# Kernel tuning notes

Measured on AMD Instinct MI355X. Metric: run time of the kernel, lower is better.

The kernel has to match this reference:

```python
import jax, jax.numpy as jnp
import numpy as np

Nu, Nd = 40000, 20000          # users, drugs
FIN, HID, H = 128, 256, 4      # input feat, hidden_dim, heads
D = HID // H                   # per-head dim (64)
HAN_OUT, HD = 64, 16           # HANConv out_channels, per-head dim
E, ER = 80000, 80000           # edges per relation (main / refined graph)


def _seg_softmax(a, seg, num):
    # segment softmax over destination index, stable
    m = jax.ops.segment_max(a, seg, num_segments=num)
    ex = jnp.exp(a - m[seg])
    s = jax.ops.segment_sum(ex, seg, num_segments=num)
    return ex / (s[seg] + 1e-16)


def setup_inputs():
    key = jax.random.key(0)
    ks = iter(jax.random.split(key, 80))
    def nrm(shape, scale=0.05):
        return jax.random.normal(next(ks), shape, jnp.float32) * scale
    def edges(ns, nd, e):
        src = jax.random.randint(next(ks), (e,), 0, ns)
        dst = jax.random.randint(next(ks), (e,), 0, nd)
        return jnp.stack([src, dst]).astype(jnp.int32)
    return {
        'x_user': nrm((Nu, FIN), 1.0), 'x_drug': nrm((Nd, FIN), 1.0),
        'x_user_ref': nrm((Nu, FIN), 1.0),
        'ei_ud': edges(Nu, Nd, E), 'ei_du': edges(Nd, Nu, E), 'ei_uu': edges(Nu, Nu, E),
        'ei_r1': edges(Nu, Nu, ER), 'ei_r2': edges(Nu, Nu, ER),
        # HANConv params (refined graph, user-only)
        'W_han': nrm((FIN, HAN_OUT)), 'b_han': jnp.zeros((HAN_OUT,), jnp.float32),
        'a_src_r1': nrm((H, HD)), 'a_dst_r1': nrm((H, HD)),
        'a_src_r2': nrm((H, HD)), 'a_dst_r2': nrm((H, HD)),
        'Wk_sem': nrm((HAN_OUT, HAN_OUT)), 'bk_sem': jnp.zeros((HAN_OUT,), jnp.float32),
        'q_sem': nrm((HAN_OUT,)),
        # per-node-type input linears
        'W_in_user': nrm((FIN, HID)), 'b_in_user': jnp.zeros((HID,), jnp.float32),
        'W_in_drug': nrm((FIN, HID)), 'b_in_drug': jnp.zeros((HID,), jnp.float32),
        # HGTConv params
        'W_kqv_user': nrm((HID, 3 * HID)), 'b_kqv_user': jnp.zeros((3 * HID,), jnp.float32),
        'W_kqv_drug': nrm((HID, 3 * HID)), 'b_kqv_drug': jnp.zeros((3 * HID,), jnp.float32),
        'Wk_ud': nrm((H, D, D), 0.1), 'Wv_ud': nrm((H, D, D), 0.1), 'p_ud': jnp.ones((H,), jnp.float32),
        'Wk_du': nrm((H, D, D), 0.1), 'Wv_du': nrm((H, D, D), 0.1), 'p_du': jnp.ones((H,), jnp.float32),
        'Wk_uu': nrm((H, D, D), 0.1), 'Wv_uu': nrm((H, D, D), 0.1), 'p_uu': jnp.ones((H,), jnp.float32),
        'W_out_user': nrm((HID, HID)), 'b_out_user': jnp.zeros((HID,), jnp.float32),
        'W_out_drug': nrm((HID, HID)), 'b_out_drug': jnp.zeros((HID,), jnp.float32),
        'skip_user': jnp.array(1.0, jnp.float32), 'skip_drug': jnp.array(1.0, jnp.float32),
        # final fusion linear
        'W_fin': nrm((HID + HAN_OUT, HID)), 'b_fin': jnp.zeros((HID,), jnp.float32),
    }


def reference(x_user, x_drug, x_user_ref, ei_ud, ei_du, ei_uu, ei_r1, ei_r2,
              W_han, b_han, a_src_r1, a_dst_r1, a_src_r2, a_dst_r2,
              Wk_sem, bk_sem, q_sem,
              W_in_user, b_in_user, W_in_drug, b_in_drug,
              W_kqv_user, b_kqv_user, W_kqv_drug, b_kqv_drug,
              Wk_ud, Wv_ud, p_ud, Wk_du, Wv_du, p_du, Wk_uu, Wv_uu, p_uu,
              W_out_user, b_out_user, W_out_drug, b_out_drug,
              skip_user, skip_drug, W_fin, b_fin):
    # ---------- HANConv on refined graph (two user-user meta-paths) ----------
    h = (x_user_ref @ W_han + b_han).reshape(Nu, H, HD)
    outs = []
    for ei, a_s, a_d in ((ei_r1, a_src_r1, a_dst_r1), (ei_r2, a_src_r2, a_dst_r2)):
        s, d = ei[0], ei[1]
        al_s = (h * a_s).sum(-1)                      # [Nu,H]
        al_d = (h * a_d).sum(-1)
        al = jax.nn.leaky_relu(al_s[s] + al_d[d], 0.2)  # [ER,H]
        al = _seg_softmax(al, d, Nu)
        o = jax.ops.segment_sum(h[s] * al[:, :, None], d, num_segments=Nu)
        outs.append(jax.nn.relu(o.reshape(Nu, HAN_OUT)))
    outs = jnp.stack(outs)                            # [2,Nu,64]
    score = (q_sem * jnp.tanh(outs @ Wk_sem + bk_sem).mean(axis=1)).sum(-1)  # [2]
    sem = jax.nn.softmax(score, axis=0)
    x_ref_out = (sem[:, None, None] * outs).sum(0)    # [Nu,64]

    # ---------- per-node-type input projection + relu ----------
    xu = jax.nn.relu(x_user @ W_in_user + b_in_user)
    xd = jax.nn.relu(x_drug @ W_in_drug + b_in_drug)

    # ---------- HGTConv ----------
    kqv_u = xu @ W_kqv_user + b_kqv_user
    kqv_d = xd @ W_kqv_drug + b_kqv_drug
    ku, qu, vu = [t.reshape(-1, H, D) for t in jnp.split(kqv_u, 3, axis=1)]
    kd, qd, vd = [t.reshape(-1, H, D) for t in jnp.split(kqv_d, 3, axis=1)]
    q_all = jnp.concatenate([qu, qd], axis=0)         # dst offsets: user=0, drug=Nu
    src_feat = {'user': (ku, vu), 'drug': (kd, vd)}
    dst_off = {'user': 0, 'drug': Nu}
    edge_types = [('user', 'drug', ei_ud, Wk_ud, Wv_ud, p_ud),
                  ('drug', 'user', ei_du, Wk_du, Wv_du, p_du),
                  ('user', 'user', ei_uu, Wk_uu, Wv_uu, p_uu)]
    scale = 1.0 / np.sqrt(D).astype(np.float32)
    alphas, vals, dsts = [], [], []
    for st, dt, ei, Wk, Wv, p in edge_types:
        k_src, v_src = src_feat[st]
        kp = jnp.einsum('nhd,hde->nhe', k_src, Wk)    # relation-specific per-head transform
        vp = jnp.einsum('nhd,hde->nhe', v_src, Wv)
        s, d = ei[0], ei[1]
        gd = d + dst_off[dt]
        a = (q_all[gd] * kp[s]).sum(-1) * p[None, :] * scale  # [E,H]
        alphas.append(a); vals.append(vp[s]); dsts.append(gd)
    a = jnp.concatenate(alphas)
    v = jnp.concatenate(vals)
    gd = jnp.concatenate(dsts)
    a = _seg_softmax(a, gd, Nu + Nd)                  # softmax over all in-edges of each dst
    out = jax.ops.segment_sum(v * a[:, :, None], gd, num_segments=Nu + Nd)
    out = out.reshape(Nu + Nd, HID)
    ou, od = out[:Nu], out[Nu:]
    ou = jax.nn.gelu(ou, approximate=False) @ W_out_user + b_out_user
    od = jax.nn.gelu(od, approximate=False) @ W_out_drug + b_out_drug
    su = jax.nn.sigmoid(skip_user)
    sd = jax.nn.sigmoid(skip_drug)
    ou = su * ou + (1.0 - su) * xu
    od = sd * od + (1.0 - sd) * xd                    # drug branch (kept for fidelity)
    # ---------- fuse HGT user embedding with HAN refined embedding ----------
    x_emb = jnp.concatenate([ou, x_ref_out], axis=1) @ W_fin + b_fin
    return x_emb
```

## Files before the change

kernel.cpp:

```cpp
#include <hip/hip_runtime.h>
#include <hip/hip_bf16.h>

#define NU 40000
#define ND 20000
#define NUP 40192
#define NDP 20224
#define HIDC 256
#define NHEAD 4
#define NEDGE 80000
#define CHUNK 2048
#define NCH 20
#define AL4 (NU * 4)

typedef __attribute__((ext_vector_type(8))) short bf16x8;
typedef __attribute__((ext_vector_type(8))) unsigned short u16x8;
typedef __attribute__((ext_vector_type(4))) float f32x4;

static __device__ __forceinline__ float b2f(unsigned short u) {
  union { unsigned int u; float f; } x; x.u = (unsigned int)u << 16; return x.f;
}
static __device__ __forceinline__ unsigned short f2b(float f) {
  union { float f; unsigned int u; } x; x.f = f;
  unsigned int r = x.u + 0x7FFFu + ((x.u >> 16) & 1u);
  return (unsigned short)(r >> 16);
}

static __device__ __forceinline__ void gload_lds16(const void* g, void* l) {
  __builtin_amdgcn_global_load_lds((const __attribute__((address_space(1))) unsigned int*)g,
                                   (__attribute__((address_space(3))) unsigned int*)l, 16, 0, 0);
}

template<int ACT>
__global__ __launch_bounds__(512)
void gemm_bf16(const unsigned short* __restrict__ A,
               const unsigned short* __restrict__ Bt,
               const float* __restrict__ bias,
               float* __restrict__ Cf, int ldcf,
               unsigned short* __restrict__ Cb, int ldcb,
               int M, int N, int K, int Mblk,
               const float* __restrict__ skipp,
               const unsigned short* __restrict__ xprev,
               int halfRows,
               const unsigned short* __restrict__ Bt2,
               const float* __restrict__ bias2, int M2,
               const float* __restrict__ as1, const float* __restrict__ ad1,
               const float* __restrict__ as2, const float* __restrict__ ad2,
               float* __restrict__ alsd)
{
  __shared__ __attribute__((aligned(128))) unsigned char smem[49152];
  unsigned short* ldsA = (unsigned short*)smem;
  unsigned short* ldsB = ldsA + 16384;
  float* ldsE = (float*)smem;

  const int Nx = (N + 127) >> 7;
  const int S = Nx << 3;
  const int flat = blockIdx.x;
  const int jj = flat % S, kq = flat / S;
  const int bx = jj >> 3, by = (kq << 3) + (jj & 7);
  if (by >= Mblk) return;

  const int tid  = threadIdx.x;
  const int lane = tid & 63, wv = tid >> 6;
  const int row0 = by * 256, col0 = bx * 128;

  const unsigned short* Btu = Bt;
  const float* biasu = bias;
  int Mu = M;
  int cfoff = 0;
  if (row0 >= halfRows) { Btu = Bt2; biasu = bias2; Mu = M2; cfoff = 64; }

  const int rl = lane >> 3;
  const int sS = (lane & 7) ^ rl;

  const int lr = lane & 15, lk = lane >> 4;
  const int wr = wv >> 1, wc = wv & 1;
  const int swz = lr & 7;

  f32x4 acc[4][4] = {};

  for (int k0 = 0; k0 < K; k0 += 64) {
#pragma unroll
    for (int i = 0; i < 4; i++) {
      size_t ga = (size_t)(row0 + wv * 32 + i * 8 + rl) * K + k0 + sS * 8;
      gload_lds16(A + ga, ldsA + wv * 2048 + i * 512);
    }
#pragma unroll
    for (int i = 0; i < 2; i++) {
      size_t gb = (size_t)(col0 + wv * 16 + i * 8 + rl) * K + k0 + sS * 8;
      gload_lds16(Btu + gb, ldsB + wv * 1024 + i * 512);
    }
    __syncthreads();
#pragma unroll
    for (int half = 0; half < 2; half++) {
      const int k8 = half * 4 + lk;
      const int so = (k8 ^ swz) << 3;
      bf16x8 av[4], bv[4];
#pragma unroll
      for (int m = 0; m < 4; m++)
        av[m] = *(const bf16x8*)&ldsA[(wr * 64 + m * 16 + lr) * 64 + so];
#pragma unroll
      for (int n = 0; n < 4; n++)
        bv[n] = *(const bf16x8*)&ldsB[(wc * 64 + n * 16 + lr) * 64 + so];
#pragma unroll
      for (int m = 0; m < 4; m++)
#pragma unroll
        for (int n = 0; n < 4; n++)
          acc[m][n] = __builtin_amdgcn_mfma_f32_16x16x32_bf16(av[m], bv[n], acc[m][n], 0, 0, 0);
    }
    __syncthreads();
  }

  if (ACT == 2) {
    __shared__ float csum[64];
    if (tid < 64) csum[tid] = 0.f;
    __syncthreads();
#pragma unroll
    for (int n = 0; n < 4; n++) {
      int col = col0 + wc * 64 + n * 16 + lr;
      if (col < N) {
        float bi = biasu[col];
        float local = 0.f;
#pragma unroll
        for (int m = 0; m < 4; m++)
#pragma unroll
          for (int g = 0; g < 4; g++) {
            int row = row0 + wr * 64 + m * 16 + lk * 4 + g;
            if (row < Mu) local += tanhf(acc[m][n][g] + bi);
          }
        atomicAdd(&csum[col], local);
      }
    }
    __syncthreads();
    if (tid < 64) atomicAdd(&Cf[cfoff + tid], csum[tid]);
    return;
  }

  float su = 0.f;
  if (ACT == 3) su = 1.f / (1.f + expf(-skipp[0]));
  float bi[4];
#pragma unroll
  for (int n = 0; n < 4; n++) {
    int col = col0 + wc * 64 + n * 16 + lr;
    bi[n] = (col < N) ? biasu[col] : 0.f;
  }

#pragma unroll
  for (int ch = 0; ch < 4; ch++) {
    __syncthreads();
    if (wr == ch) {
#pragma unroll
      for (int m = 0; m < 4; m++)
#pragma unroll
        for (int n = 0; n < 4; n++) {
          int c = wc * 64 + n * 16 + lr;
          int wbase = c + 2 * (c >> 5);
#pragma unroll
          for (int g = 0; g < 4; g++) {
            int lrow = m * 16 + lk * 4 + g;
            ldsE[lrow * 134 + wbase] = acc[m][n][g] + bi[n];
          }
        }
    }
    __syncthreads();
#pragma unroll
    for (int i = 0; i < 2; i++) {
      int c = tid + i * 512;
      int lrow = c >> 4, cc = c & 15;
      int row = row0 + ch * 64 + lrow;
      int colb = cc * 8;
      int base = lrow * 134 + 8 * cc + 2 * (cc >> 2);
      float v[8];
#pragma unroll
      for (int q2 = 0; q2 < 4; q2++) {
        float2 tv = *(const float2*)&ldsE[base + 2 * q2];
        v[2 * q2] = tv.x; v[2 * q2 + 1] = tv.y;
      }
      if (ACT == 1) {
#pragma unroll
        for (int q = 0; q < 8; q++) v[q] = fmaxf(v[q], 0.f);
      }
      if (ACT == 3) {
        u16x8 xp = *(const u16x8*)(xprev + (size_t)row * 256 + col0 + colb);
#pragma unroll
        for (int q = 0; q < 8; q++) v[q] = su * v[q] + (1.f - su) * b2f(xp[q]);
      }
      if (ACT == 4) {
        if (colb < 64 && row < Mu) {
          int hh = colb >> 4;
          int o0 = colb & 15;
          float s1 = 0, d1 = 0, s2 = 0, d2 = 0;
#pragma unroll
          for (int q = 0; q < 8; q++) {
            float x = v[q];
            s1 += x * as1[hh * 16 + o0 + q];
            d1 += x * ad1[hh * 16 + o0 + q];
            s2 += x * as2[hh * 16 + o0 + q];
            d2 += x * ad2[hh * 16 + o0 + q];
          }
          s1 += __shfl_xor(s1, 1); d1 += __shfl_xor(d1, 1);
          s2 += __shfl_xor(s2, 1); d2 += __shfl_xor(d2, 1);
          if ((lane & 1) == 0) {
            size_t idx = (size_t)row * 4 + hh;
            alsd[idx]           = s1;
            alsd[AL4 + idx]     = d1;
            alsd[2 * AL4 + idx] = s2;
            alsd[3 * AL4 + idx] = d2;
          }
        }
      }
      if (Cb) {
        u16x8 o;
#pragma unroll
        for (int q = 0; q < 8; q++) o[q] = f2b(row < Mu ? v[q] : 0.f);
        *(u16x8*)(Cb + (size_t)row * ldcb + col0 + colb) = o;
      }
      if (Cf && row < Mu) {
        int col = col0 + colb;
        if (col < N)
          *(float4*)&Cf[(size_t)row * ldcf + col] = make_float4(v[0], v[1], v[2], v[3]);
        if (col + 4 < N)
          *(float4*)&Cf[(size_t)row * ldcf + col + 4] = make_float4(v[4], v[5], v[6], v[7]);
      }
    }
  }
}

__global__ __launch_bounds__(256)
void prep_all(const float* __restrict__ x_user, const float* __restrict__ x_drug,
              const float* __restrict__ x_user_ref,
              const float* __restrict__ W_in_user, const float* __restrict__ W_in_drug,
              const float* __restrict__ W_kqv_user, const float* __restrict__ W_kqv_drug,
              const float* __restrict__ W_out_user, const float* __restrict__ W_fin,
              const float* __restrict__ W_han, const float* __restrict__ Wk_sem,
              const float* __restrict__ Wk_uu, const float* __restrict__ Wv_uu,
              const float* __restrict__ Wk_du, const float* __restrict__ Wv_du,
              const float* __restrict__ b_kqv_user, const float* __restrict__ b_kqv_drug,
              unsigned short* __restrict__ xub, unsigned short* __restrict__ xdb,
              unsigned short* __restrict__ xrb,
              unsigned short* __restrict__ Btu_in, unsigned short* __restrict__ Btd_in,
              unsigned short* __restrict__ Btall_u, unsigned short* __restrict__ Btall_d,
              unsigned short* __restrict__ Bto, unsigned short* __restrict__ Btf,
              unsigned short* __restrict__ Bth, unsigned short* __restrict__ BtWk,
              float* __restrict__ ball_u, float* __restrict__ ball_d,
              int* __restrict__ cnt)
{
  __shared__ float sWh[4096];
  __shared__ float sWk[64][65];
  const int b = blockIdx.x;
  const int tid = threadIdx.x;

  if (b < 16) {
    int mat = b >> 2, hh = b & 3;
    const float* Wkqv; const float* Wh; unsigned short* Bt; int coloff;
    switch (mat) {
      case 0:  Wkqv = W_kqv_user; Wh = Wk_uu; Bt = Btall_u;          coloff = 0;   break;
      case 1:  Wkqv = W_kqv_user; Wh = Wv_uu; Bt = Btall_u + 131072; coloff = 512; break;
      case 2:  Wkqv = W_kqv_drug; Wh = Wk_du; Bt = Btall_d;          coloff = 0;   break;
      default: Wkqv = W_kqv_drug; Wh = Wv_du; Bt = Btall_d + 65536;  coloff = 512; break;
    }
    for (int i = tid; i < 4096; i += 256) sWh[i] = Wh[hh * 4096 + i];
    __syncthreads();
    for (int ct = 0; ct < 4; ct++) {
      for (int i = tid; i < 4096; i += 256) {
        int cl = i >> 6, d = i & 63;
        sWk[cl][d] = Wkqv[(size_t)(ct * 64 + cl) * 768 + coloff + hh * 64 + d];
      }
      __syncthreads();
      int cl = tid & 63, eg = tid >> 6;
      float acc[16] = {};
      for (int d = 0; d < 64; d++) {
        float w = sWk[cl][d];
#pragma unroll
        for (int e = 0; e < 16; e++) acc[e] += w * sWh[d * 64 + eg * 16 + e];
      }
#pragma unroll
      for (int e = 0; e < 16; e++)
        Bt[(size_t)(hh * 64 + eg * 16 + e) * 256 + ct * 64 + cl] = f2b(acc[e]);
      __syncthreads();
    }
    return;
  }
  if (b < 21) {
    int j = (b - 16) * 256 + tid;
    const float* bb; const float* Wh; float* outp; int coloff, e256;
    if (j < 256)       { outp = &ball_u[j];        bb = b_kqv_user; Wh = Wk_uu; coloff = 0;   e256 = j; }
    else if (j < 512)  { ball_u[j] = b_kqv_user[j]; return; }
    else if (j < 768)  { outp = &ball_u[j];        bb = b_kqv_user; Wh = Wv_uu; coloff = 512; e256 = j - 512; }
    else if (j < 1024) { outp = &ball_d[j - 768];  bb = b_kqv_drug; Wh = Wk_du; coloff = 0;   e256 = j - 768; }
    else               { outp = &ball_d[j - 768];  bb = b_kqv_drug; Wh = Wv_du; coloff = 512; e256 = j - 1024; }
    int hh = e256 >> 6, e = e256 & 63;
    float acc = 0.f;
    for (int d = 0; d < 64; d++)
      acc += bb[coloff + hh * 64 + d] * Wh[hh * 4096 + d * 64 + e];
    *outp = acc;
    return;
  }
  if (b < 139) {
    int u = (b - 21) * 256 + tid;
    int idx = u * 4;
    if (idx < 3 * NU) *(int4*)&cnt[idx] = make_int4(0, 0, 0, 0);
    return;
  }
  if (b < 1323) {
    size_t i = (size_t)(b - 139) * 256 + tid;
    const float* W; unsigned short* Bt; int ldw, coloff, K, N;
    if (i < 32768)       { W = W_in_user;  Bt = Btu_in;          ldw = 256; coloff = 0;   K = 128; N = 256; }
    else if (i < 65536)  { W = W_in_drug;  Bt = Btd_in;          ldw = 256; coloff = 0;   K = 128; N = 256; i -= 32768; }
    else if (i < 131072) { W = W_kqv_user; Bt = Btall_u + 65536; ldw = 768; coloff = 256; K = 256; N = 256; i -= 65536; }
    else if (i < 196608) { W = W_out_user; Bt = Bto;             ldw = 256; coloff = 0;   K = 256; N = 256; i -= 131072; }
    else if (i < 278528) { W = W_fin;      Bt = Btf;             ldw = 256; coloff = 0;   K = 320; N = 256; i -= 196608; }
    else if (i < 294912) { W = W_han;      Bt = Bth;             ldw = 64;  coloff = 0;   K = 128; N = 64;  i -= 278528; }
    else                 { W = Wk_sem;     Bt = BtWk;            ldw = 64;  coloff = 0;   K = 64;  N = 64;  i -= 294912; }
    int n = (int)(i / K), k = (int)(i - (size_t)n * K);
    Bt[i] = (n < N) ? f2b(W[(size_t)k * ldw + coloff + n]) : 0;
    return;
  }
  {
    int bc = b - 1323;
    const float* in; unsigned short* outp; int M; int bl;
    if (bc < 2512)      { in = x_user;     outp = xub; M = NU; bl = bc; }
    else if (bc < 3776) { in = x_drug;     outp = xdb; M = ND; bl = bc - 2512; }
    else                { in = x_user_ref; outp = xrb; M = NU; bl = bc - 3776; }
    size_t e0 = ((size_t)bl * 256 + tid) * 8;
    int r = (int)(e0 >> 7);
    u16x8 o;
    if (r < M) {
      float4 a = *(const float4*)(in + e0);
      float4 bb = *(const float4*)(in + e0 + 4);
      o[0] = f2b(a.x); o[1] = f2b(a.y); o[2] = f2b(a.z); o[3] = f2b(a.w);
      o[4] = f2b(bb.x); o[5] = f2b(bb.y); o[6] = f2b(bb.z); o[7] = f2b(bb.w);
    } else {
#pragma unroll
      for (int q = 0; q < 8; q++) o[q] = 0;
    }
    *(u16x8*)(outp + e0) = o;
  }
}

__global__ void hist_all(const int* __restrict__ ei_du, const int* __restrict__ ei_uu,
                         const int* __restrict__ ei_r1, const int* __restrict__ ei_r2,
                         int* __restrict__ cnt)
{
  int t = blockIdx.x * 256 + threadIdx.x;
  if (t >= NEDGE) return;
  const int* ei; int* c;
  switch (blockIdx.y) {
    case 0: ei = ei_du; c = cnt; break;
    case 1: ei = ei_uu; c = cnt; break;
    case 2: ei = ei_r1; c = cnt + NU; break;
    default: ei = ei_r2; c = cnt + 2 * NU; break;
  }
  atomicAdd(&c[ei[NEDGE + t]], 1);
}

__global__ __launch_bounds__(256)
void scan_partial(const int* __restrict__ cnt, int* __restrict__ csums)
{
  int b = blockIdx.x;
  int rel = b / NCH, ch = b - rel * NCH;
  const int* c = cnt + (size_t)rel * NU;
  int t = threadIdx.x;
  int i0 = ch * CHUNK + t * 8;
  int s = 0;
#pragma unroll
  for (int j = 0; j < 8; j++) { int i = i0 + j; if (i < NU) s += c[i]; }
  __shared__ int ps[256];
  ps[t] = s;
  __syncthreads();
  for (int d = 128; d > 0; d >>= 1) { if (t < d) ps[t] += ps[t + d]; __syncthreads(); }
  if (t == 0) csums[b] = ps[0];
}

__global__ void scan_mid(const int* __restrict__ csums, int* __restrict__ coffs,
                         int* __restrict__ rs, float* __restrict__ colpart2)
{
  int r = threadIdx.x;
  if (r < 128) colpart2[r] = 0.f;
  if (r >= 3) return;
  int run = 0;
  for (int ch = 0; ch < NCH; ch++) { coffs[r * NCH + ch] = run; run += csums[r * NCH + ch]; }
  rs[(size_t)r * NUP + NU] = run;
}

__global__ __launch_bounds__(256)
void scan_final(int* __restrict__ cnt, const int* __restrict__ coffs,
                int* __restrict__ rs)
{
  int b = blockIdx.x;
  int rel = b / NCH, ch = b - rel * NCH;
  int* c = cnt + (size_t)rel * NU;
  int* r = rs + (size_t)rel * NUP;
  int t = threadIdx.x;
  int i0 = ch * CHUNK + t * 8;
  int loc[8]; int s = 0;
#pragma unroll
  for (int j = 0; j < 8; j++) {
    int i = i0 + j;
    loc[j] = (i < NU) ? c[i] : 0;
    if (i < NU) c[i] = 0;
    s += loc[j];
  }
  __shared__ int ps[256];
  ps[t] = s;
  __syncthreads();
  for (int d = 1; d < 256; d <<= 1) {
    int o = (t >= d) ? ps[t - d] : 0;
    __syncthreads();
    ps[t] += o;
    __syncthreads();
  }
  int run = coffs[b] + ps[t] - s;
#pragma unroll
  for (int j = 0; j < 8; j++) { int i = i0 + j; if (i < NU) { r[i] = run; run += loc[j]; } }
}

__global__ void han_fill2(const int* __restrict__ ei1, const int* __restrict__ ei2,
                          const float* __restrict__ alsd,
                          const int* __restrict__ rs, int* __restrict__ cur,
                          int* __restrict__ esrc1, float* __restrict__ aev1,
                          int* __restrict__ esrc2, float* __restrict__ aev2)
{
  int t = blockIdx.x * 256 + threadIdx.x;
  if (t >= NEDGE * 4) return;
  int y = blockIdx.y;
  const int* ei = y ? ei2 : ei1;
  const float* als = alsd + (y ? 2 * AL4 : 0);
  const float* ald = alsd + (y ? 3 * AL4 : AL4);
  const int* rsp = rs + (size_t)(y ? 2 : 1) * NUP;
  int* curp = cur + (size_t)(y ? 2 : 1) * NU;
  int* esrc = y ? esrc2 : esrc1;
  float* aev = y ? aev2 : aev1;
  int e = t >> 2, hh = t & 3;
  int s = ei[e], d = ei[NEDGE + e];
  float al = als[s * 4 + hh] + ald[d * 4 + hh];
  al = (al >= 0.f) ? al : 0.2f * al;
  float ex = expf(al);
  int pos = 0;
  if (hh == 0) pos = rsp[d] + atomicAdd(&curp[d], 1);
  pos = __shfl(pos, (threadIdx.x & 63) & ~3, 64);
  aev[pos * 4 + hh] = ex;
  if (hh == 0) esrc[pos] = s;
}

__global__ __launch_bounds__(256)
void han_gather2(const int* __restrict__ rs,
                 const int* __restrict__ esrc1, const float* __restrict__ aev1,
                 const int* __restrict__ esrc2, const float* __restrict__ aev2,
                 const float* __restrict__ h,
                 unsigned short* __restrict__ obf1, unsigned short* __restrict__ obf2)
{
  int gid = blockIdx.x * 256 + threadIdx.x;
  int wid = gid >> 6, lane = gid & 63;
  if (wid >= NUP) return;
  int y = blockIdx.y;
  const int* rsp = rs + (size_t)(y ? 2 : 1) * NUP;
  const int* esrc = y ? esrc2 : esrc1;
  const float* aev = y ? aev2 : aev1;
  unsigned short* obf = y ? obf2 : obf1;
  int head = lane >> 4;
  int beg = 0, end = 0;
  if (wid < NU) { beg = rsp[wid]; end = rsp[wid + 1]; }
  float asum = 0.f;
  for (int i = beg; i < end; i++) asum += aev[i * 4 + head];
  float inv = 1.f / (asum + 1e-16f);
  float a = 0.f;
  for (int i = beg; i < end; i++)
    a += aev[i * 4 + head] * inv * h[(size_t)esrc[i] * 64 + lane];
  obf[(size_t)wid * 64 + lane] = f2b(fmaxf(a, 0.f));
}

__global__ void sem_final2(const float* __restrict__ colpart2,
                           const float* __restrict__ q_sem, float* __restrict__ semv)
{
  int t = threadIdx.x;
  int j = t & 63;
  __shared__ float sv[128];
  sv[t] = colpart2[t] * q_sem[j] * (1.0f / NU);
  __syncthreads();
  if (t == 0) {
    float s0 = 0, s1 = 0;
    for (int i = 0; i < 64; i++) { s0 += sv[i]; s1 += sv[64 + i]; }
    float m = fmaxf(s0, s1);
    float e0 = expf(s0 - m), e1 = expf(s1 - m);
    semv[0] = e0 / (e0 + e1); semv[1] = e1 / (e0 + e1);
  }
}

__global__ void hgt_fill2(const int* __restrict__ ei_du, const int* __restrict__ ei_uu,
                          const unsigned short* __restrict__ qb,
                          const unsigned short* __restrict__ kvdb,
                          const float* __restrict__ p_du, const float* __restrict__ p_uu,
                          const int* __restrict__ rs, int* __restrict__ cur,
                          int* __restrict__ esrc, float* __restrict__ aev)
{
  int t = blockIdx.x * 256 + threadIdx.x;
  if (t >= NEDGE * 4) return;
  int y = blockIdx.y;
  const int* ei = y ? ei_uu : ei_du;
  const unsigned short* kb = y ? qb : kvdb;
  const int ks = y ? 768 : 512;
  const int voff = y ? 512 : NUP * 768 + 256;
  const float* p = y ? p_uu : p_du;
  int e = t >> 2, hh = t & 3;
  int s = ei[e], d = ei[NEDGE + e];
  const uint4* qv = (const uint4*)(qb + (size_t)d * 768 + 256 + hh * 64);
  const uint4* kv = (const uint4*)(kb + (size_t)s * ks + hh * 64);
  float acc = 0.f;
#pragma unroll
  for (int i = 0; i < 8; i++) {
    uint4 a = qv[i], b = kv[i];
    unsigned int aw[4] = {a.x, a.y, a.z, a.w};
    unsigned int bw[4] = {b.x, b.y, b.z, b.w};
#pragma unroll
    for (int u = 0; u < 4; u++) {
      acc += b2f((unsigned short)(aw[u] & 0xffff)) * b2f((unsigned short)(bw[u] & 0xffff));
      acc += b2f((unsigned short)(aw[u] >> 16))    * b2f((unsigned short)(bw[u] >> 16));
    }
  }
  float ex = expf(acc * p[hh] * 0.125f);
  int pos = 0;
  if (hh == 0) pos = rs[d] + atomicAdd(&cur[d], 1);
  pos = __shfl(pos, (threadIdx.x & 63) & ~3, 64);
  aev[pos * 4 + hh] = ex;
  if (hh == 0) esrc[pos] = voff + s * ks;
}

__global__ __launch_bounds__(256)
void hgt_gather(const int* __restrict__ rs, const int* __restrict__ esrc,
                const float* __restrict__ aev, const unsigned short* __restrict__ vbase,
                unsigned short* __restrict__ houtb)
{
  int gid = blockIdx.x * 256 + threadIdx.x;
  int wid = gid >> 6, lane = gid & 63;
  if (wid >= NUP) return;
  int head = lane >> 4;
  int beg = 0, end = 0;
  if (wid < NU) { beg = rs[wid]; end = rs[wid + 1]; }
  float asum = 0.f;
  for (int i = beg; i < end; i++) asum += aev[i * 4 + head];
  float inv = 1.f / (asum + 1e-16f);
  float a0 = 0, a1 = 0, a2 = 0, a3 = 0;
  for (int i = beg; i < end; i++) {
    float w = aev[i * 4 + head] * inv;
    const ushort4 v = *(const ushort4*)(vbase + (size_t)esrc[i] + lane * 4);
    a0 += b2f(v.x) * w; a1 += b2f(v.y) * w; a2 += b2f(v.z) * w; a3 += b2f(v.w) * w;
  }
  ushort4 o;
  o.x = f2b(0.5f * a0 * (1.f + erff(a0 * 0.70710678118654752f)));
  o.y = f2b(0.5f * a1 * (1.f + erff(a1 * 0.70710678118654752f)));
  o.z = f2b(0.5f * a2 * (1.f + erff(a2 * 0.70710678118654752f)));
  o.w = f2b(0.5f * a3 * (1.f + erff(a3 * 0.70710678118654752f)));
  *(ushort4*)(houtb + (size_t)wid * 256 + lane * 4) = o;
}

__global__ void fill_ref_b(const unsigned short* __restrict__ obf1,
                           const unsigned short* __restrict__ obf2,
                           const float* __restrict__ semv, unsigned short* __restrict__ afinb)
{
  int t = blockIdx.x * 256 + threadIdx.x;
  if (t >= NUP * 64) return;
  int n = t >> 6, j = t & 63;
  float v = semv[0] * b2f(obf1[t]) + semv[1] * b2f(obf2[t]);
  afinb[(size_t)n * 320 + 256 + j] = f2b(v);
}

extern "C" void kernel_launch(void* const* d_in, const int* in_sizes, int n_in,
                              void* d_out, int out_size, void* d_ws, size_t ws_size,
                              hipStream_t stream)
{
  (void)in_sizes; (void)n_in; (void)out_size; (void)ws_size;
  const float* x_user     = (const float*)d_in[0];
  const float* x_drug     = (const float*)d_in[1];
  const float* x_user_ref = (const float*)d_in[2];
  const int*   ei_du      = (const int*)d_in[4];
  const int*   ei_uu      = (const int*)d_in[5];
  const int*   ei_r1      = (const int*)d_in[6];
  const int*   ei_r2      = (const int*)d_in[7];
  const float* W_han      = (const float*)d_in[8];
  const float* b_han      = (const float*)d_in[9];
  const float* a_src_r1   = (const float*)d_in[10];
  const float* a_dst_r1   = (const float*)d_in[11];
  const float* a_src_r2   = (const float*)d_in[12];
  const float* a_dst_r2   = (const float*)d_in[13];
  const float* Wk_sem     = (const float*)d_in[14];
  const float* bk_sem     = (const float*)d_in[15];
  const float* q_sem      = (const float*)d_in[16];
  const float* W_in_user  = (const float*)d_in[17];
  const float* b_in_user  = (const float*)d_in[18];
  const float* W_in_drug  = (const float*)d_in[19];
  const float* b_in_drug  = (const float*)d_in[20];
  const float* W_kqv_user = (const float*)d_in[21];
  const float* b_kqv_user = (const float*)d_in[22];
  const float* W_kqv_drug = (const float*)d_in[23];
  const float* b_kqv_drug = (const float*)d_in[24];
  const float* Wk_du      = (const float*)d_in[28];
  const float* Wv_du      = (const float*)d_in[29];
  const float* p_du       = (const float*)d_in[30];
  const float* Wk_uu      = (const float*)d_in[31];
  const float* Wv_uu      = (const float*)d_in[32];
  const float* p_uu       = (const float*)d_in[33];
  const float* W_out_user = (const float*)d_in[34];
  const float* b_out_user = (const float*)d_in[35];
  const float* skip_user  = (const float*)d_in[38];
  const float* W_fin      = (const float*)d_in[40];
  const float* b_fin      = (const float*)d_in[41];
  float* out = (float*)d_out;

  char* base = (char*)d_ws;
  size_t off = 0;
  auto alloc = [&](size_t bytes) { char* p = base + off; off += (bytes + 255) & ~(size_t)255; return p; };

  float* h       = (float*)alloc((size_t)NU * 64 * 4);
  float* alsd    = (float*)alloc((size_t)4 * AL4 * 4);
  float* colpart2= (float*)alloc(128 * 4);
  float* semv    = (float*)alloc(64);
  float* ball_u  = (float*)alloc(768 * 4);
  float* ball_d  = (float*)alloc(512 * 4);

  int* cnt   = (int*)alloc((size_t)3 * NU * 4);
  int* rs    = (int*)alloc((size_t)3 * NUP * 4);
  int* csums = (int*)alloc((size_t)3 * NCH * 4);
  int* coffs = (int*)alloc((size_t)3 * NCH * 4);
  int* esrcH = (int*)alloc((size_t)2 * NEDGE * 4);
  float* aevH= (float*)alloc((size_t)2 * NEDGE * 4 * 4);
  int* esrc1 = (int*)alloc((size_t)NEDGE * 4);
  float* aev1= (float*)alloc((size_t)NEDGE * 4 * 4);
  int* esrc2 = (int*)alloc((size_t)NEDGE * 4);
  float* aev2= (float*)alloc((size_t)NEDGE * 4 * 4);

  unsigned short* obf1 = (unsigned short*)alloc((size_t)NUP * 64 * 2);
  unsigned short* obf2 = (unsigned short*)alloc((size_t)NUP * 64 * 2);

  unsigned short* qukvb = (unsigned short*)alloc((size_t)NUP * 768 * 2);
  unsigned short* kvdb  = (unsigned short*)alloc((size_t)NDP * 512 * 2);

  unsigned short* xub2d = (unsigned short*)alloc((size_t)NUP * 256 * 2);
  unsigned short* xdb2d = (unsigned short*)alloc((size_t)NDP * 256 * 2);

  unsigned short* houtb = (unsigned short*)alloc((size_t)NUP * 256 * 2);
  unsigned short* xrb   = houtb;

  unsigned short* afinb = (unsigned short*)alloc((size_t)NUP * 320 * 2);
  unsigned short* xub   = afinb;
  unsigned short* xdb   = afinb + (size_t)NUP * 128;

  unsigned short* Btu_in  = (unsigned short*)alloc(256 * 128 * 2);
  unsigned short* Btd_in  = (unsigned short*)alloc(256 * 128 * 2);
  unsigned short* Btall_u = (unsigned short*)alloc(768 * 256 * 2);
  unsigned short* Btall_d = (unsigned short*)alloc(512 * 256 * 2);
  unsigned short* Bto     = (unsigned short*)alloc(256 * 256 * 2);
  unsigned short* Btf     = (unsigned short*)alloc(256 * 320 * 2);
  unsigned short* Bth     = (unsigned short*)alloc(128 * 128 * 2);
  unsigned short* BtWk    = (unsigned short*)alloc(128 * 64 * 2);

  dim3 blk(256), blk5(512);
  auto g1 = [](size_t n) { return dim3((unsigned)((n + 255) / 256)); };
  auto gg = [](int N, int Mblk) {
    int Nx = (N + 127) / 128;
    return dim3((unsigned)(((Mblk + 7) / 8) * 8 * Nx));
  };
  const int BIG = 1 << 30;
  const unsigned short* NB = nullptr;
  const float* NF = nullptr;

  const int prep_blocks = 16 + 5 + 118 + 1184 + 6288;
  prep_all<<<dim3(prep_blocks), blk, 0, stream>>>(
      x_user, x_drug, x_user_ref, W_in_user, W_in_drug, W_kqv_user, W_kqv_drug,
      W_out_user, W_fin, W_han, Wk_sem, Wk_uu, Wv_uu, Wk_du, Wv_du,
      b_kqv_user, b_kqv_drug,
      xub, xdb, xrb, Btu_in, Btd_in, Btall_u, Btall_d, Bto, Btf, Bth, BtWk,
      ball_u, ball_d, cnt);

  hist_all<<<dim3((NEDGE + 255) / 256, 4), blk, 0, stream>>>(ei_du, ei_uu, ei_r1, ei_r2, cnt);
  scan_partial<<<3 * NCH, blk, 0, stream>>>(cnt, csums);
  scan_mid<<<1, 128, 0, stream>>>(csums, coffs, rs, colpart2);
  scan_final<<<3 * NCH, blk, 0, stream>>>(cnt, coffs, rs);

  gemm_bf16<4><<<gg(64, 157), blk5, 0, stream>>>(
      xrb, Bth, b_han, h, 64, (unsigned short*)nullptr, 0, NU, 64, 128, 157,
      nullptr, nullptr, BIG, NB, NF, 0,
      a_src_r1, a_dst_r1, a_src_r2, a_dst_r2, alsd);

  han_fill2<<<dim3((NEDGE * 4 + 255) / 256, 2), blk, 0, stream>>>(
      ei_r1, ei_r2, alsd, rs, cnt, esrc1, aev1, esrc2, aev2);
  han_gather2<<<dim3((NUP * 64 + 255) / 256, 2), blk, 0, stream>>>(
      rs, esrc1, aev1, esrc2, aev2, h, obf1, obf2);

  gemm_bf16<2><<<gg(64, 314), blk5, 0, stream>>>(
      obf1, BtWk, bk_sem, colpart2, 0, (unsigned short*)nullptr, 0, NU, 64, 64, 314,
      nullptr, nullptr, NUP, BtWk, bk_sem, NUP + NU,
      NF, NF, NF, NF, nullptr);
  sem_final2<<<1, 128, 0, stream>>>(colpart2, q_sem, semv);

  gemm_bf16<1><<<gg(256, 236), blk5, 0, stream>>>(
      xub, Btu_in, b_in_user, (float*)nullptr, 0, xub2d, 256, NU, 256, 128, 236,
      nullptr, nullptr, NUP, Btd_in, b_in_drug, NUP + ND,
      NF, NF, NF, NF, nullptr);

  gemm_bf16<0><<<gg(768, 157), blk5, 0, stream>>>(
      xub2d, Btall_u, ball_u, (float*)nullptr, 0, qukvb, 768, NU, 768, 256, 157,
      nullptr, nullptr, BIG, NB, NF, 0, NF, NF, NF, NF, nullptr);
  gemm_bf16<0><<<gg(512, 79), blk5, 0, stream>>>(
      xdb2d, Btall_d, ball_d, (float*)nullptr, 0, kvdb, 512, ND, 512, 256, 79,
      nullptr, nullptr, BIG, NB, NF, 0, NF, NF, NF, NF, nullptr);

  hgt_fill2<<<dim3((NEDGE * 4 + 255) / 256, 2), blk, 0, stream>>>(
      ei_du, ei_uu, qukvb, kvdb, p_du, p_uu, rs, cnt, esrcH, aevH);
  hgt_gather<<<g1((size_t)NUP * 64), blk, 0, stream>>>(rs, esrcH, aevH, qukvb, houtb);

  gemm_bf16<3><<<gg(256, 157), blk5, 0, stream>>>(
      houtb, Bto, b_out_user, (float*)nullptr, 0, afinb, 320, NU, 256, 256, 157,
      skip_user, xub2d, BIG, NB, NF, 0, NF, NF, NF, NF, nullptr);
  fill_ref_b<<<g1((size_t)NUP * 64), blk, 0, stream>>>(obf1, obf2, semv, afinb);

  gemm_bf16<0><<<gg(256, 157), blk5, 0, stream>>>(
      afinb, Btf, b_fin, out, 256, (unsigned short*)nullptr, 0, NU, 256, 320, 157,
      nullptr, nullptr, BIG, NB, NF, 0, NF, NF, NF, NF, nullptr);
}
```

Measured before the change: 302.6 us.

## Merge user/drug KQV GEMMs and fuse HAN/HGT fill and gather kernels

The user and drug KQV projection GEMMs now run in one grouped launch: blocks beyond the first grid's count switch to the second problem's pointers and sizes. The HAN and HGT edge-fill kernels are merged into one 4-slice launch, and their gather kernels into one 3-slice launch. The semantic GEMM is moved after the gathers. This cuts the number of kernel launches and lets independent work share the GPU instead of running one small grid after another. In exchange the GEMM carries extra parameters and branches, and the merged kernels have divergent per-slice paths.

```diff
diff --git a/kernel.cpp b/kernel.cpp
--- a/kernel.cpp
+++ b/kernel.cpp
@@ -45,27 +45,45 @@
                const float* __restrict__ bias2, int M2,
                const float* __restrict__ as1, const float* __restrict__ ad1,
                const float* __restrict__ as2, const float* __restrict__ ad2,
-               float* __restrict__ alsd)
+               float* __restrict__ alsd,
+               int B1,
+               const unsigned short* __restrict__ A_r2,
+               const unsigned short* __restrict__ Bt_r2,
+               const float* __restrict__ bias_r2,
+               unsigned short* __restrict__ Cb_r2, int ldcb_r2,
+               int M_r2, int N_r2, int Mblk_r2)
 {
   __shared__ __attribute__((aligned(128))) unsigned char smem[49152];
   unsigned short* ldsA = (unsigned short*)smem;
   unsigned short* ldsB = ldsA + 16384;
   float* ldsE = (float*)smem;
 
-  const int Nx = (N + 127) >> 7;
+  int flat = blockIdx.x;
+  const unsigned short* Ap = A;
+  const unsigned short* Btp = Bt;
+  const float* biasp = bias;
+  float* Cfp = Cf;
+  unsigned short* Cbp = Cb;
+  int ldcbp = ldcb, Mp = M, Np = N, Mblkp = Mblk;
+  if (flat >= B1) {
+    flat -= B1;
+    Ap = A_r2; Btp = Bt_r2; biasp = bias_r2; Cbp = Cb_r2; ldcbp = ldcb_r2;
+    Mp = M_r2; Np = N_r2; Mblkp = Mblk_r2; Cfp = nullptr;
+  }
+
+  const int Nx = (Np + 127) >> 7;
   const int S = Nx << 3;
-  const int flat = blockIdx.x;
   const int jj = flat % S, kq = flat / S;
   const int bx = jj >> 3, by = (kq << 3) + (jj & 7);
-  if (by >= Mblk) return;
+  if (by >= Mblkp) return;
 
   const int tid  = threadIdx.x;
   const int lane = tid & 63, wv = tid >> 6;
   const int row0 = by * 256, col0 = bx * 128;
 
-  const unsigned short* Btu = Bt;
-  const float* biasu = bias;
-  int Mu = M;
+  const unsigned short* Btu = Btp;
+  const float* biasu = biasp;
+  int Mu = Mp;
   int cfoff = 0;
   if (row0 >= halfRows) { Btu = Bt2; biasu = bias2; Mu = M2; cfoff = 64; }
 
@@ -82,7 +100,7 @@
 #pragma unroll
     for (int i = 0; i < 4; i++) {
       size_t ga = (size_t)(row0 + wv * 32 + i * 8 + rl) * K + k0 + sS * 8;
-      gload_lds16(A + ga, ldsA + wv * 2048 + i * 512);
+      gload_lds16(Ap + ga, ldsA + wv * 2048 + i * 512);
     }
 #pragma unroll
     for (int i = 0; i < 2; i++) {
@@ -117,7 +135,7 @@
 #pragma unroll
     for (int n = 0; n < 4; n++) {
       int col = col0 + wc * 64 + n * 16 + lr;
-      if (col < N) {
+      if (col < Np) {
         float bi = biasu[col];
         float local = 0.f;
 #pragma unroll
@@ -131,7 +149,7 @@
       }
     }
     __syncthreads();
-    if (tid < 64) atomicAdd(&Cf[cfoff + tid], csum[tid]);
+    if (tid < 64) atomicAdd(&Cfp[cfoff + tid], csum[tid]);
     return;
   }
 
@@ -141,7 +159,7 @@
 #pragma unroll
   for (int n = 0; n < 4; n++) {
     int col = col0 + wc * 64 + n * 16 + lr;
-    bi[n] = (col < N) ? biasu[col] : 0.f;
+    bi[n] = (col < Np) ? biasu[col] : 0.f;
   }
 
 #pragma unroll
@@ -208,18 +226,18 @@
           }
         }
       }
-      if (Cb) {
+      if (Cbp) {
         u16x8 o;
 #pragma unroll
         for (int q = 0; q < 8; q++) o[q] = f2b(row < Mu ? v[q] : 0.f);
-        *(u16x8*)(Cb + (size_t)row * ldcb + col0 + colb) = o;
-      }
-      if (Cf && row < Mu) {
+        *(u16x8*)(Cbp + (size_t)row * ldcbp + col0 + colb) = o;
+      }
+      if (Cfp && row < Mu) {
         int col = col0 + colb;
-        if (col < N)
-          *(float4*)&Cf[(size_t)row * ldcf + col] = make_float4(v[0], v[1], v[2], v[3]);
-        if (col + 4 < N)
-          *(float4*)&Cf[(size_t)row * ldcf + col + 4] = make_float4(v[4], v[5], v[6], v[7]);
+        if (col < Np)
+          *(float4*)&Cfp[(size_t)row * ldcf + col] = make_float4(v[0], v[1], v[2], v[3]);
+        if (col + 4 < Np)
+          *(float4*)&Cfp[(size_t)row * ldcf + col + 4] = make_float4(v[4], v[5], v[6], v[7]);
       }
     }
   }
@@ -414,59 +432,117 @@
   for (int j = 0; j < 8; j++) { int i = i0 + j; if (i < NU) { r[i] = run; run += loc[j]; } }
 }
 
-__global__ void han_fill2(const int* __restrict__ ei1, const int* __restrict__ ei2,
-                          const float* __restrict__ alsd,
-                          const int* __restrict__ rs, int* __restrict__ cur,
-                          int* __restrict__ esrc1, float* __restrict__ aev1,
-                          int* __restrict__ esrc2, float* __restrict__ aev2)
+__global__ void fill_all(const int* __restrict__ ei_r1, const int* __restrict__ ei_r2,
+                         const int* __restrict__ ei_du, const int* __restrict__ ei_uu,
+                         const float* __restrict__ alsd,
+                         const unsigned short* __restrict__ qb,
+                         const unsigned short* __restrict__ kvdb,
+                         const float* __restrict__ p_du, const float* __restrict__ p_uu,
+                         const int* __restrict__ rs, int* __restrict__ cur,
+                         int* __restrict__ esrc1, float* __restrict__ aev1,
+                         int* __restrict__ esrc2, float* __restrict__ aev2,
+                         int* __restrict__ esrcH, float* __restrict__ aevH)
 {
   int t = blockIdx.x * 256 + threadIdx.x;
   if (t >= NEDGE * 4) return;
   int y = blockIdx.y;
-  const int* ei = y ? ei2 : ei1;
-  const float* als = alsd + (y ? 2 * AL4 : 0);
-  const float* ald = alsd + (y ? 3 * AL4 : AL4);
-  const int* rsp = rs + (size_t)(y ? 2 : 1) * NUP;
-  int* curp = cur + (size_t)(y ? 2 : 1) * NU;
-  int* esrc = y ? esrc2 : esrc1;
-  float* aev = y ? aev2 : aev1;
   int e = t >> 2, hh = t & 3;
-  int s = ei[e], d = ei[NEDGE + e];
-  float al = als[s * 4 + hh] + ald[d * 4 + hh];
-  al = (al >= 0.f) ? al : 0.2f * al;
-  float ex = expf(al);
-  int pos = 0;
-  if (hh == 0) pos = rsp[d] + atomicAdd(&curp[d], 1);
-  pos = __shfl(pos, (threadIdx.x & 63) & ~3, 64);
-  aev[pos * 4 + hh] = ex;
-  if (hh == 0) esrc[pos] = s;
+  if (y < 2) {
+    const int* ei = y ? ei_r2 : ei_r1;
+    const float* als = alsd + (y ? 2 * AL4 : 0);
+    const float* ald = alsd + (y ? 3 * AL4 : AL4);
+    const int* rsp = rs + (size_t)(y ? 2 : 1) * NUP;
+    int* curp = cur + (size_t)(y ? 2 : 1) * NU;
+    int* esrc = y ? esrc2 : esrc1;
+    float* aev = y ? aev2 : aev1;
+    int s = ei[e], d = ei[NEDGE + e];
+    float al = als[s * 4 + hh] + ald[d * 4 + hh];
+    al = (al >= 0.f) ? al : 0.2f * al;
+    float ex = expf(al);
+    int pos = 0;
+    if (hh == 0) pos = rsp[d] + atomicAdd(&curp[d], 1);
+    pos = __shfl(pos, (threadIdx.x & 63) & ~3, 64);
+    aev[pos * 4 + hh] = ex;
+    if (hh == 0) esrc[pos] = s;
+  } else {
+    int yy = y - 2;
+    const int* ei = yy ? ei_uu : ei_du;
+    const unsigned short* kb = yy ? qb : kvdb;
+    const int ks = yy ? 768 : 512;
+    const int voff = yy ? 512 : NUP * 768 + 256;
+    const float* p = yy ? p_uu : p_du;
+    int s = ei[e], d = ei[NEDGE + e];
+    const uint4* qv = (const uint4*)(qb + (size_t)d * 768 + 256 + hh * 64);
+    const uint4* kv = (const uint4*)(kb + (size_t)s * ks + hh * 64);
+    float acc = 0.f;
+#pragma unroll
+    for (int i = 0; i < 8; i++) {
+      uint4 a = qv[i], b = kv[i];
+      unsigned int aw[4] = {a.x, a.y, a.z, a.w};
+      unsigned int bw[4] = {b.x, b.y, b.z, b.w};
+#pragma unroll
+      for (int u = 0; u < 4; u++) {
+        acc += b2f((unsigned short)(aw[u] & 0xffff)) * b2f((unsigned short)(bw[u] & 0xffff));
+        acc += b2f((unsigned short)(aw[u] >> 16))    * b2f((unsigned short)(bw[u] >> 16));
+      }
+    }
+    float ex = expf(acc * p[hh] * 0.125f);
+    int pos = 0;
+    if (hh == 0) pos = rs[d] + atomicAdd(&cur[d], 1);
+    pos = __shfl(pos, (threadIdx.x & 63) & ~3, 64);
+    aevH[pos * 4 + hh] = ex;
+    if (hh == 0) esrcH[pos] = voff + s * ks;
+  }
 }
 
 __global__ __launch_bounds__(256)
-void han_gather2(const int* __restrict__ rs,
-                 const int* __restrict__ esrc1, const float* __restrict__ aev1,
-                 const int* __restrict__ esrc2, const float* __restrict__ aev2,
-                 const float* __restrict__ h,
-                 unsigned short* __restrict__ obf1, unsigned short* __restrict__ obf2)
+void gather_all(const int* __restrict__ rs,
+                const int* __restrict__ esrc1, const float* __restrict__ aev1,
+                const int* __restrict__ esrc2, const float* __restrict__ aev2,
+                const int* __restrict__ esrcH, const float* __restrict__ aevH,
+                const float* __restrict__ h,
+                const unsigned short* __restrict__ vbase,
+                unsigned short* __restrict__ obf1, unsigned short* __restrict__ obf2,
+                unsigned short* __restrict__ houtb)
 {
   int gid = blockIdx.x * 256 + threadIdx.x;
   int wid = gid >> 6, lane = gid & 63;
   if (wid >= NUP) return;
   int y = blockIdx.y;
-  const int* rsp = rs + (size_t)(y ? 2 : 1) * NUP;
-  const int* esrc = y ? esrc2 : esrc1;
-  const float* aev = y ? aev2 : aev1;
-  unsigned short* obf = y ? obf2 : obf1;
   int head = lane >> 4;
-  int beg = 0, end = 0;
-  if (wid < NU) { beg = rsp[wid]; end = rsp[wid + 1]; }
-  float asum = 0.f;
-  for (int i = beg; i < end; i++) asum += aev[i * 4 + head];
-  float inv = 1.f / (asum + 1e-16f);
-  float a = 0.f;
-  for (int i = beg; i < end; i++)
-    a += aev[i * 4 + head] * inv * h[(size_t)esrc[i] * 64 + lane];
-  obf[(size_t)wid * 64 + lane] = f2b(fmaxf(a, 0.f));
+  if (y < 2) {
+    const int* rsp = rs + (size_t)(y ? 2 : 1) * NUP;
+    const int* esrc = y ? esrc2 : esrc1;
+    const float* aev = y ? aev2 : aev1;
+    unsigned short* obf = y ? obf2 : obf1;
+    int beg = 0, end = 0;
+    if (wid < NU) { beg = rsp[wid]; end = rsp[wid + 1]; }
+    float asum = 0.f;
+    for (int i = beg; i < end; i++) asum += aev[i * 4 + head];
+    float inv = 1.f / (asum + 1e-16f);
+    float a = 0.f;
+    for (int i = beg; i < end; i++)
+      a += aev[i * 4 + head] * inv * h[(size_t)esrc[i] * 64 + lane];
+    obf[(size_t)wid * 64 + lane] = f2b(fmaxf(a, 0.f));
+  } else {
+    int beg = 0, end = 0;
+    if (wid < NU) { beg = rs[wid]; end = rs[wid + 1]; }
+    float asum = 0.f;
+    for (int i = beg; i < end; i++) asum += aevH[i * 4 + head];
+    float inv = 1.f / (asum + 1e-16f);
+    float a0 = 0, a1 = 0, a2 = 0, a3 = 0;
+    for (int i = beg; i < end; i++) {
+      float w = aevH[i * 4 + head] * inv;
+      const ushort4 v = *(const ushort4*)(vbase + (size_t)esrcH[i] + lane * 4);
+      a0 += b2f(v.x) * w; a1 += b2f(v.y) * w; a2 += b2f(v.z) * w; a3 += b2f(v.w) * w;
+    }
+    ushort4 o;
+    o.x = f2b(0.5f * a0 * (1.f + erff(a0 * 0.70710678118654752f)));
+    o.y = f2b(0.5f * a1 * (1.f + erff(a1 * 0.70710678118654752f)));
+    o.z = f2b(0.5f * a2 * (1.f + erff(a2 * 0.70710678118654752f)));
+    o.w = f2b(0.5f * a3 * (1.f + erff(a3 * 0.70710678118654752f)));
+    *(ushort4*)(houtb + (size_t)wid * 256 + lane * 4) = o;
+  }
 }
 
 __global__ void sem_final2(const float* __restrict__ colpart2,
@@ -484,73 +560,6 @@
     float e0 = expf(s0 - m), e1 = expf(s1 - m);
     semv[0] = e0 / (e0 + e1); semv[1] = e1 / (e0 + e1);
   }
-}
-
-__global__ void hgt_fill2(const int* __restrict__ ei_du, const int* __restrict__ ei_uu,
-                          const unsigned short* __restrict__ qb,
-                          const unsigned short* __restrict__ kvdb,
-                          const float* __restrict__ p_du, const float* __restrict__ p_uu,
-                          const int* __restrict__ rs, int* __restrict__ cur,
-                          int* __restrict__ esrc, float* __restrict__ aev)
-{
-  int t = blockIdx.x * 256 + threadIdx.x;
-  if (t >= NEDGE * 4) return;
-  int y = blockIdx.y;
-  const int* ei = y ? ei_uu : ei_du;
-  const unsigned short* kb = y ? qb : kvdb;
-  const int ks = y ? 768 : 512;
-  const int voff = y ? 512 : NUP * 768 + 256;
-  const float* p = y ? p_uu : p_du;
-  int e = t >> 2, hh = t & 3;
-  int s = ei[e], d = ei[NEDGE + e];
-  const uint4* qv = (const uint4*)(qb + (size_t)d * 768 + 256 + hh * 64);
-  const uint4* kv = (const uint4*)(kb + (size_t)s * ks + hh * 64);
-  float acc = 0.f;
-#pragma unroll
-  for (int i = 0; i < 8; i++) {
-    uint4 a = qv[i], b = kv[i];
-    unsigned int aw[4] = {a.x, a.y, a.z, a.w};
-    unsigned int bw[4] = {b.x, b.y, b.z, b.w};
-#pragma unroll
-    for (int u = 0; u < 4; u++) {
-      acc += b2f((unsigned short)(aw[u] & 0xffff)) * b2f((unsigned short)(bw[u] & 0xffff));
-      acc += b2f((unsigned short)(aw[u] >> 16))    * b2f((unsigned short)(bw[u] >> 16));
-    }
-  }
-  float ex = expf(acc * p[hh] * 0.125f);
-  int pos = 0;
-  if (hh == 0) pos = rs[d] + atomicAdd(&cur[d], 1);
-  pos = __shfl(pos, (threadIdx.x & 63) & ~3, 64);
-  aev[pos * 4 + hh] = ex;
-  if (hh == 0) esrc[pos] = voff + s * ks;
-}
-
-__global__ __launch_bounds__(256)
-void hgt_gather(const int* __restrict__ rs, const int* __restrict__ esrc,
-                const float* __restrict__ aev, const unsigned short* __restrict__ vbase,
-                unsigned short* __restrict__ houtb)
-{
-  int gid = blockIdx.x * 256 + threadIdx.x;
-  int wid = gid >> 6, lane = gid & 63;
-  if (wid >= NUP) return;
-  int head = lane >> 4;
-  int beg = 0, end = 0;
-  if (wid < NU) { beg = rs[wid]; end = rs[wid + 1]; }
-  float asum = 0.f;
-  for (int i = beg; i < end; i++) asum += aev[i * 4 + head];
-  float inv = 1.f / (asum + 1e-16f);
-  float a0 = 0, a1 = 0, a2 = 0, a3 = 0;
-  for (int i = beg; i < end; i++) {
-    float w = aev[i * 4 + head] * inv;
-    const ushort4 v = *(const ushort4*)(vbase + (size_t)esrc[i] + lane * 4);
-    a0 += b2f(v.x) * w; a1 += b2f(v.y) * w; a2 += b2f(v.z) * w; a3 += b2f(v.w) * w;
-  }
-  ushort4 o;
-  o.x = f2b(0.5f * a0 * (1.f + erff(a0 * 0.70710678118654752f)));
-  o.y = f2b(0.5f * a1 * (1.f + erff(a1 * 0.70710678118654752f)));
-  o.z = f2b(0.5f * a2 * (1.f + erff(a2 * 0.70710678118654752f)));
-  o.w = f2b(0.5f * a3 * (1.f + erff(a3 * 0.70710678118654752f)));
-  *(ushort4*)(houtb + (size_t)wid * 256 + lane * 4) = o;
 }
 
 __global__ void fill_ref_b(const unsigned short* __restrict__ obf1,
@@ -657,11 +666,12 @@
   auto g1 = [](size_t n) { return dim3((unsigned)((n + 255) / 256)); };
   auto gg = [](int N, int Mblk) {
     int Nx = (N + 127) / 128;
-    return dim3((unsigned)(((Mblk + 7) / 8) * 8 * Nx));
+    return (unsigned)(((Mblk + 7) / 8) * 8 * Nx);
   };
   const int BIG = 1 << 30;
   const unsigned short* NB = nullptr;
   const float* NF = nullptr;
+  unsigned short* NBm = nullptr;
 
   const int prep_blocks = 16 + 5 + 118 + 1184 + 6288;
   prep_all<<<dim3(prep_blocks), blk, 0, stream>>>(
@@ -677,43 +687,47 @@
   scan_final<<<3 * NCH, blk, 0, stream>>>(cnt, coffs, rs);
 
   gemm_bf16<4><<<gg(64, 157), blk5, 0, stream>>>(
-      xrb, Bth, b_han, h, 64, (unsigned short*)nullptr, 0, NU, 64, 128, 157,
+      xrb, Bth, b_han, h, 64, NBm, 0, NU, 64, 128, 157,
       nullptr, nullptr, BIG, NB, NF, 0,
-      a_src_r1, a_dst_r1, a_src_r2, a_dst_r2, alsd);
-
-  han_fill2<<<dim3((NEDGE * 4 + 255) / 256, 2), blk, 0, stream>>>(
-      ei_r1, ei_r2, alsd, rs, cnt, esrc1, aev1, esrc2, aev2);
-  han_gather2<<<dim3((NUP * 64 + 255) / 256, 2), blk, 0, stream>>>(
-      rs, esrc1, aev1, esrc2, aev2, h, obf1, obf2);
-
-  gemm_bf16<2><<<gg(64, 314), blk5, 0, stream>>>(
-      obf1, BtWk, bk_sem, colpart2, 0, (unsigned short*)nullptr, 0, NU, 64, 64, 314,
-      nullptr, nullptr, NUP, BtWk, bk_sem, NUP + NU,
-      NF, NF, NF, NF, nullptr);
-  sem_final2<<<1, 128, 0, stream>>>(colpart2, q_sem, semv);
+      a_src_r1, a_dst_r1, a_src_r2, a_dst_r2, alsd,
+      BIG, NB, NB, NF, NBm, 0, 0, 0, 0);
 
   gemm_bf16<1><<<gg(256, 236), blk5, 0, stream>>>(
       xub, Btu_in, b_in_user, (float*)nullptr, 0, xub2d, 256, NU, 256, 128, 236,
       nullptr, nullptr, NUP, Btd_in, b_in_drug, NUP + ND,
-      NF, NF, NF, NF, nullptr);
-
-  gemm_bf16<0><<<gg(768, 157), blk5, 0, stream>>>(
-      xub2d, Btall_u, ball_u, (float*)nullptr, 0, qukvb, 768, NU, 768, 256, 157,
-      nullptr, nullptr, BIG, NB, NF, 0, NF, NF, NF, NF, nullptr);
-  gemm_bf16<0><<<gg(512, 79), blk5, 0, stream>>>(
-      xdb2d, Btall_d, ball_d, (float*)nullptr, 0, kvdb, 512, ND, 512, 256, 79,
-      nullptr, nullptr, BIG, NB, NF, 0, NF, NF, NF, NF, nullptr);
-
-  hgt_fill2<<<dim3((NEDGE * 4 + 255) / 256, 2), blk, 0, stream>>>(
-      ei_du, ei_uu, qukvb, kvdb, p_du, p_uu, rs, cnt, esrcH, aevH);
-  hgt_gather<<<g1((size_t)NUP * 64), blk, 0, stream>>>(rs, esrcH, aevH, qukvb, houtb);
+      NF, NF, NF, NF, nullptr,
+      BIG, NB, NB, NF, NBm, 0, 0, 0, 0);
+
+  {
+    unsigned B1 = gg(768, 157), B2 = gg(512, 79);
+    gemm_bf16<0><<<dim3(B1 + B2), blk5, 0, stream>>>(
+        xub2d, Btall_u, ball_u, (float*)nullptr, 0, qukvb, 768, NU, 768, 256, 157,
+        nullptr, nullptr, BIG, NB, NF, 0, NF, NF, NF, NF, nullptr,
+        (int)B1, xdb2d, Btall_d, ball_d, kvdb, 512, ND, 512, 79);
+  }
+
+  fill_all<<<dim3((NEDGE * 4 + 255) / 256, 4), blk, 0, stream>>>(
+      ei_r1, ei_r2, ei_du, ei_uu, alsd, qukvb, kvdb, p_du, p_uu,
+      rs, cnt, esrc1, aev1, esrc2, aev2, esrcH, aevH);
+
+  gather_all<<<dim3((NUP * 64 + 255) / 256, 3), blk, 0, stream>>>(
+      rs, esrc1, aev1, esrc2, aev2, esrcH, aevH, h, qukvb, obf1, obf2, houtb);
+
+  gemm_bf16<2><<<gg(64, 314), blk5, 0, stream>>>(
+      obf1, BtWk, bk_sem, colpart2, 0, NBm, 0, NU, 64, 64, 314,
+      nullptr, nullptr, NUP, BtWk, bk_sem, NUP + NU,
+      NF, NF, NF, NF, nullptr,
+      BIG, NB, NB, NF, NBm, 0, 0, 0, 0);
+  sem_final2<<<1, 128, 0, stream>>>(colpart2, q_sem, semv);
 
   gemm_bf16<3><<<gg(256, 157), blk5, 0, stream>>>(
       houtb, Bto, b_out_user, (float*)nullptr, 0, afinb, 320, NU, 256, 256, 157,
-      skip_user, xub2d, BIG, NB, NF, 0, NF, NF, NF, NF, nullptr);
+      skip_user, xub2d, BIG, NB, NF, 0, NF, NF, NF, NF, nullptr,
+      BIG, NB, NB, NF, NBm, 0, 0, 0, 0);
   fill_ref_b<<<g1((size_t)NUP * 64), blk, 0, stream>>>(obf1, obf2, semv, afinb);
 
   gemm_bf16<0><<<gg(256, 157), blk5, 0, stream>>>(
-      afinb, Btf, b_fin, out, 256, (unsigned short*)nullptr, 0, NU, 256, 320, 157,
-      nullptr, nullptr, BIG, NB, NF, 0, NF, NF, NF, NF, nullptr);
-}
+      afinb, Btf, b_fin, out, 256, NBm, 0, NU, 256, 320, 157,
+      nullptr, nullptr, BIG, NB, NF, 0, NF, NF, NF, NF, nullptr,
+      BIG, NB, NB, NF, NBm, 0, 0, 0, 0);
+}
```

Measured after the change: 289.0 us. 1.05x faster.
